# Performance work log

Measured on AMD Instinct MI355X. Metric: run time of the kernel, lower is better.

Reference implementation:

```python
import jax, jax.numpy as jnp
import numpy as np
from jax import lax

LAG, K, DIM, HEADS, HID, CLASSES = 8192, 4, 1024, 16, 5, 2
PRICE = 9 - K  # cat((output[k], prices)) must have length 9 (LSTM input_size)


def setup_inputs() -> dict:
    key = jax.random.key(0)
    ks = jax.random.split(key, 30)
    n = lambda i, shape, s=1.0: jax.random.normal(ks[i], shape, jnp.float32) * s
    w = 0.02  # weight init scale for stability
    return {
        "text": n(0, (LAG, K, DIM)),
        "prices": n(1, (LAG, PRICE)),
        "pos_embed": n(2, (LAG, K, DIM), w),
        "Wq1": n(3, (DIM, DIM), w), "Wk1": n(4, (DIM, DIM), w),
        "Wv1": n(5, (DIM, DIM), w), "Wo1": n(6, (DIM, DIM), w),
        "ln_g": jnp.ones((DIM,), jnp.float32), "ln_b": jnp.zeros((DIM,), jnp.float32),
        "W1": n(7, (DIM, DIM), w), "b1": jnp.zeros((DIM,), jnp.float32),
        "W2": n(8, (DIM, DIM), w), "b2": jnp.zeros((DIM,), jnp.float32),
        "Wq2": n(9, (DIM, DIM), w), "Wk2": n(10, (DIM, DIM), w),
        "Wv2": n(11, (DIM, DIM), w), "Wo2": n(12, (DIM, DIM), w),
        "w_u": n(13, (DIM, DIM)), "w_m": n(14, (DIM,)),
        "Wih": n(15, (4 * HID, 9), 0.3), "Whh": n(16, (4 * HID, HID), 0.3),
        "bih": jnp.zeros((4 * HID,), jnp.float32), "bhh": jnp.zeros((4 * HID,), jnp.float32),
        "Wt": n(17, (9 + HID, CLASSES), 0.3), "bt": jnp.zeros((CLASSES,), jnp.float32),
        "Wa": n(18, (9 + HID, CLASSES), 0.3), "ba": jnp.zeros((CLASSES,), jnp.float32),
    }


def _mha(x, Wq, Wk, Wv, Wo, h):
    # x: [lag, k, d]; batched multi-head self-attention over the k axis
    L, k, d = x.shape
    dh = d // h
    q = (x @ Wq).reshape(L, k, h, dh)
    kk = (x @ Wk).reshape(L, k, h, dh)
    v = (x @ Wv).reshape(L, k, h, dh)
    s = jnp.einsum('lqhd,lkhd->lhqk', q, kk) / jnp.sqrt(jnp.float32(dh))
    a = jax.nn.softmax(s, axis=-1)
    o = jnp.einsum('lhqk,lkhd->lqhd', a, v).reshape(L, k, d)
    return o @ Wo


def _layernorm(x, g, b, eps=1e-5):
    mu = jnp.mean(x, axis=-1, keepdims=True)
    var = jnp.mean(jnp.square(x - mu), axis=-1, keepdims=True)
    return (x - mu) * lax.rsqrt(var + eps) * g + b


def reference(text, prices, pos_embed, Wq1, Wk1, Wv1, Wo1, ln_g, ln_b,
              W1, b1, W2, b2, Wq2, Wk2, Wv2, Wo2, w_u, w_m,
              Wih, Whh, bih, bhh, Wt, bt, Wa, ba):
    # input[0] += pos_embed, then per-tweet textEncoder -- vectorized over lag
    x = text + pos_embed                                   # [lag, k, d]
    inter = _mha(x, Wq1, Wk1, Wv1, Wo1, HEADS)             # multi-head attn
    y = _layernorm(inter + x, ln_g, ln_b)                  # residual + LN
    ffn = jax.nn.relu(y @ W1 + b1) @ W2 + b2               # FFN
    m = _mha(ffn, Wq2, Wk2, Wv2, Wo2, 1)                   # single-head attn -> [lag, k, d]
    # inter = softmax(w_u^T @ tanh(w_m)) is constant across the loop
    att = jax.nn.softmax(w_u.T @ jnp.tanh(w_m), axis=0)    # [d]
    out_k = jnp.einsum('lkd,d->lk', m, att)                # [lag, k]
    lstm_in = jnp.concatenate([out_k, prices], axis=1)     # [lag, 9]

    # single-layer LSTM (pytorch gate order i, f, g, o), h0 = c0 = 0
    def step(carry, xt):
        h, c = carry
        g = xt @ Wih.T + h @ Whh.T + bih + bhh
        i, f, gg, o = jnp.split(g, 4)
        c = jax.nn.sigmoid(f) * c + jax.nn.sigmoid(i) * jnp.tanh(gg)
        h = jax.nn.sigmoid(o) * jnp.tanh(c)
        return (h, c), h

    init = (jnp.zeros((HID,), lstm_in.dtype), jnp.zeros((HID,), lstm_in.dtype))
    _, hs = lax.scan(step, init, lstm_in)                  # [lag, 5]

    feat = jnp.concatenate([lstm_in, hs], axis=1)          # [lag, 14]
    final = feat @ Wt + bt                                 # [lag, num_classes]
    auxiliary = feat @ Wa + ba                             # [lag, num_classes]
    return final, auxiliary
```

## Files before the change

kernel.cpp:

```cpp
#include <hip/hip_runtime.h>
#include <hip/hip_bf16.h>
#include <math.h>

#define LAG   8192
#define NROW  32768
#define DIMD  1024

typedef __attribute__((ext_vector_type(8))) short  short8;
typedef __attribute__((ext_vector_type(4))) float  f32x4;
typedef __attribute__((ext_vector_type(2))) float  f32x2;
typedef unsigned short ushort_t;
typedef unsigned int   uint_t;

__device__ __forceinline__ uint_t split2_pack(float f) {
    unsigned u = __float_as_uint(f);
    unsigned r = u + 0x7FFFu + ((u >> 16) & 1u);
    unsigned h = r >> 16;
    float hf = __uint_as_float(h << 16);
    float lf = f - hf;
    unsigned u2 = __float_as_uint(lf);
    unsigned r2 = u2 + 0x7FFFu + ((u2 >> 16) & 1u);
    return h | (r2 & 0xFFFF0000u);
}
__device__ __forceinline__ float updp(uint_t p) {
    return __uint_as_float(p << 16) + __uint_as_float(p & 0xFFFF0000u);
}

__device__ __forceinline__ void unpack16(const uint_t* r, uint4& h0, uint4& h1,
                                         uint4& l0, uint4& l1) {
    h0.x = __builtin_amdgcn_perm(r[1],  r[0],  0x05040100u);
    h0.y = __builtin_amdgcn_perm(r[3],  r[2],  0x05040100u);
    h0.z = __builtin_amdgcn_perm(r[5],  r[4],  0x05040100u);
    h0.w = __builtin_amdgcn_perm(r[7],  r[6],  0x05040100u);
    h1.x = __builtin_amdgcn_perm(r[9],  r[8],  0x05040100u);
    h1.y = __builtin_amdgcn_perm(r[11], r[10], 0x05040100u);
    h1.z = __builtin_amdgcn_perm(r[13], r[12], 0x05040100u);
    h1.w = __builtin_amdgcn_perm(r[15], r[14], 0x05040100u);
    l0.x = __builtin_amdgcn_perm(r[1],  r[0],  0x07060302u);
    l0.y = __builtin_amdgcn_perm(r[3],  r[2],  0x07060302u);
    l0.z = __builtin_amdgcn_perm(r[5],  r[4],  0x07060302u);
    l0.w = __builtin_amdgcn_perm(r[7],  r[6],  0x07060302u);
    l1.x = __builtin_amdgcn_perm(r[9],  r[8],  0x07060302u);
    l1.y = __builtin_amdgcn_perm(r[11], r[10], 0x07060302u);
    l1.z = __builtin_amdgcn_perm(r[13], r[12], 0x07060302u);
    l1.w = __builtin_amdgcn_perm(r[15], r[14], 0x07060302u);
}

template<int BM, int CM, bool BIAS, bool RELU>
__global__ __launch_bounds__(256) void mgemm(
    const uint_t* __restrict__ Apk, const void* __restrict__ Bsrc,
    const float* __restrict__ bias,
    float* __restrict__ Cf, uint_t* __restrict__ Cp)
{
    __shared__ ushort_t As_h[128*40], As_l[128*40], Bs_h[128*40], Bs_l[128*40];
    const int tid  = threadIdx.x;
    const int lane = tid & 63;
    const int wave = tid >> 6;
    const int wm   = (wave & 1) * 64;
    const int wn   = (wave >> 1) * 64;
    const int ln15 = lane & 15;
    const int q8   = (lane >> 4) * 8;
    const int lin  = blockIdx.y * 8 + blockIdx.x;
    const int swz  = (lin & 7) * gridDim.y + (lin >> 3);
    const int row0 = (swz >> 3) * 128;
    const int col0 = (swz & 7) * 128;

    const int ar  = tid >> 1;
    const int ako = (tid & 1) << 4;
    const int bn  = tid & 127;
    const int bk  = (tid >> 7) << 4;

    f32x4 acc[4][4] = {};

    uint_t a_r[16] __attribute__((aligned(16)));
    uint_t b_r[16] __attribute__((aligned(16)));

    {
        const uint_t* Apt = Apk + (size_t)(row0 + ar) * DIMD + ako;
        *(uint4*)&a_r[0]  = *(const uint4*)(Apt + 0);
        *(uint4*)&a_r[4]  = *(const uint4*)(Apt + 4);
        *(uint4*)&a_r[8]  = *(const uint4*)(Apt + 8);
        *(uint4*)&a_r[12] = *(const uint4*)(Apt + 12);
        if constexpr (BM == 1) {
            const uint_t* Bpt = (const uint_t*)Bsrc + (size_t)bk * DIMD + col0 + bn;
            #pragma unroll
            for (int i = 0; i < 16; ++i) b_r[i] = Bpt[(size_t)i * DIMD];
        } else {
            const float* Bpt = (const float*)Bsrc + (size_t)bk * DIMD + col0 + bn;
            #pragma unroll
            for (int i = 0; i < 16; ++i) b_r[i] = split2_pack(Bpt[(size_t)i * DIMD]);
        }
    }

    for (int k0 = 0; k0 < DIMD; k0 += 32) {
        __syncthreads();
        {
            uint4 h0, h1, l0, l1;
            unpack16(a_r, h0, h1, l0, l1);
            *(uint4*)&As_h[ar*40 + ako]     = h0;
            *(uint4*)&As_h[ar*40 + ako + 8] = h1;
            *(uint4*)&As_l[ar*40 + ako]     = l0;
            *(uint4*)&As_l[ar*40 + ako + 8] = l1;
            unpack16(b_r, h0, h1, l0, l1);
            *(uint4*)&Bs_h[bn*40 + bk]      = h0;
            *(uint4*)&Bs_h[bn*40 + bk + 8]  = h1;
            *(uint4*)&Bs_l[bn*40 + bk]      = l0;
            *(uint4*)&Bs_l[bn*40 + bk + 8]  = l1;
        }
        __syncthreads();

        if (k0 + 32 < DIMD) {
            const int kn = k0 + 32;
            const uint_t* Apt = Apk + (size_t)(row0 + ar) * DIMD + kn + ako;
            *(uint4*)&a_r[0]  = *(const uint4*)(Apt + 0);
            *(uint4*)&a_r[4]  = *(const uint4*)(Apt + 4);
            *(uint4*)&a_r[8]  = *(const uint4*)(Apt + 8);
            *(uint4*)&a_r[12] = *(const uint4*)(Apt + 12);
            if constexpr (BM == 1) {
                const uint_t* Bpt = (const uint_t*)Bsrc + (size_t)(kn + bk) * DIMD + col0 + bn;
                #pragma unroll
                for (int i = 0; i < 16; ++i) b_r[i] = Bpt[(size_t)i * DIMD];
            } else {
                const float* Bpt = (const float*)Bsrc + (size_t)(kn + bk) * DIMD + col0 + bn;
                #pragma unroll
                for (int i = 0; i < 16; ++i) b_r[i] = split2_pack(Bpt[(size_t)i * DIMD]);
            }
        }

        short8 fah[4], fal[4];
        #pragma unroll
        for (int i = 0; i < 4; ++i) {
            fah[i] = *(const short8*)&As_h[(wm + 16*i + ln15)*40 + q8];
            fal[i] = *(const short8*)&As_l[(wm + 16*i + ln15)*40 + q8];
        }
        #pragma unroll
        for (int j = 0; j < 4; ++j) {
            short8 fbh = *(const short8*)&Bs_h[(wn + 16*j + ln15)*40 + q8];
            short8 fbl = *(const short8*)&Bs_l[(wn + 16*j + ln15)*40 + q8];
            #pragma unroll
            for (int i = 0; i < 4; ++i) {
                acc[i][j] = __builtin_amdgcn_mfma_f32_16x16x32_bf16(fal[i], fbh, acc[i][j], 0, 0, 0);
                acc[i][j] = __builtin_amdgcn_mfma_f32_16x16x32_bf16(fah[i], fbl, acc[i][j], 0, 0, 0);
                acc[i][j] = __builtin_amdgcn_mfma_f32_16x16x32_bf16(fah[i], fbh, acc[i][j], 0, 0, 0);
            }
        }
    }

    #pragma unroll
    for (int j = 0; j < 4; ++j) {
        const int col = col0 + wn + 16*j + ln15;
        float bv = 0.f;
        if constexpr (BIAS) bv = bias[col];
        #pragma unroll
        for (int i = 0; i < 4; ++i) {
            #pragma unroll
            for (int r = 0; r < 4; ++r) {
                const int row = row0 + wm + 16*i + (lane >> 4)*4 + r;
                float v = acc[i][j][r] + bv;
                if constexpr (RELU) v = fmaxf(v, 0.f);
                if constexpr (CM == 0) Cf[(size_t)row*DIMD + col] = v;
                else                   Cp[(size_t)row*DIMD + col] = split2_pack(v);
            }
        }
    }
}

template<bool TRANS_B>
__global__ __launch_bounds__(256) void gemm_f32(
    const float* __restrict__ A, const float* __restrict__ B, float* __restrict__ C)
{
    __shared__ float As[16][132];
    __shared__ float Bs[16][132];
    const int tid  = threadIdx.x;
    const int tx   = tid & 15;
    const int ty   = tid >> 4;
    const int row0 = blockIdx.y * 128;
    const int col0 = blockIdx.x * 128;

    float acc[8][8];
    #pragma unroll
    for (int i = 0; i < 8; ++i)
        #pragma unroll
        for (int j = 0; j < 8; ++j) acc[i][j] = 0.f;

    for (int k0 = 0; k0 < DIMD; k0 += 16) {
        #pragma unroll
        for (int t = 0; t < 2; ++t) {
            int i  = tid + t * 256;
            int arr = i >> 2, ak = (i & 3) << 2;
            float4 av = *(const float4*)(A + (size_t)(row0 + arr) * DIMD + k0 + ak);
            As[ak + 0][arr] = av.x; As[ak + 1][arr] = av.y;
            As[ak + 2][arr] = av.z; As[ak + 3][arr] = av.w;
            if constexpr (TRANS_B) {
                float4 bv4 = *(const float4*)(B + (size_t)(col0 + arr) * DIMD + k0 + ak);
                Bs[ak + 0][arr] = bv4.x; Bs[ak + 1][arr] = bv4.y;
                Bs[ak + 2][arr] = bv4.z; Bs[ak + 3][arr] = bv4.w;
            } else {
                int br = i >> 5, bc = (i & 31) << 2;
                *(float4*)&Bs[br][bc] =
                    *(const float4*)(B + (size_t)(k0 + br) * DIMD + col0 + bc);
            }
        }
        __syncthreads();
        #pragma unroll
        for (int kk = 0; kk < 16; ++kk) {
            float a[8], b[8];
            *(float4*)&a[0] = *(const float4*)&As[kk][ty * 8];
            *(float4*)&a[4] = *(const float4*)&As[kk][ty * 8 + 4];
            *(float4*)&b[0] = *(const float4*)&Bs[kk][tx * 4];
            *(float4*)&b[4] = *(const float4*)&Bs[kk][64 + tx * 4];
            #pragma unroll
            for (int i = 0; i < 8; ++i)
                #pragma unroll
                for (int j = 0; j < 8; ++j)
                    acc[i][j] = fmaf(a[i], b[j], acc[i][j]);
        }
        __syncthreads();
    }
    #pragma unroll
    for (int i = 0; i < 8; ++i) {
        size_t rr = (size_t)(row0 + ty * 8 + i) * DIMD;
        *(float4*)(C + rr + col0 + tx * 4)      = *(float4*)&acc[i][0];
        *(float4*)(C + rr + col0 + 64 + tx * 4) = *(float4*)&acc[i][4];
    }
}

__global__ __launch_bounds__(256) void mv_kernel(
    const float* __restrict__ W, const float* __restrict__ x,
    float* __restrict__ y)
{
    const int row  = blockIdx.x * 4 + (threadIdx.x >> 6);
    const int lane = threadIdx.x & 63;
    float a = 0.f;
    #pragma unroll
    for (int c = 0; c < 16; ++c) {
        int off = c * 64 + lane;
        a = fmaf(W[(size_t)row * DIMD + off], x[off], a);
    }
    #pragma unroll
    for (int d = 1; d < 64; d <<= 1) a += __shfl_xor(a, d);
    if (lane == 0) y[row] = a;
}

__global__ __launch_bounds__(1024) void mvt_part_kernel(
    const float* __restrict__ W, const float* __restrict__ x,
    float* __restrict__ part)
{
    const int b   = blockIdx.x;
    const int tid = threadIdx.x;
    float a = 0.f;
    #pragma unroll 4
    for (int j = b * 64; j < b * 64 + 64; ++j)
        a = fmaf(W[(size_t)j * DIMD + tid], x[j], a);
    part[(size_t)b * DIMD + tid] = a;
}
__global__ __launch_bounds__(256) void mvt_red_kernel(
    const float* __restrict__ part, float* __restrict__ y)
{
    const int i = blockIdx.x * 256 + threadIdx.x;
    float s = 0.f;
    #pragma unroll
    for (int c = 0; c < 16; ++c) s += part[(size_t)c * DIMD + i];
    y[i] = s;
}

__global__ __launch_bounds__(1024) void dot_kernel(
    const float* __restrict__ a, const float* __restrict__ b,
    float* __restrict__ out)
{
    __shared__ float red[16];
    const int tid = threadIdx.x;
    float p = a[tid] * b[tid];
    #pragma unroll
    for (int d = 1; d < 64; d <<= 1) p += __shfl_xor(p, d);
    if ((tid & 63) == 0) red[tid >> 6] = p;
    __syncthreads();
    if (tid < 16) {
        float x = red[tid];
        #pragma unroll
        for (int d = 1; d < 16; d <<= 1) x += __shfl_xor(x, d);
        if (tid == 0) out[0] = x;
    }
}

__global__ __launch_bounds__(256) void splitw_kernel(
    const float* __restrict__ in, uint_t* __restrict__ out)
{
    const size_t i = ((size_t)blockIdx.x * 256 + threadIdx.x) * 4;
    float4 v = *(const float4*)(in + i);
    uint4 o;
    o.x = split2_pack(v.x); o.y = split2_pack(v.y);
    o.z = split2_pack(v.z); o.w = split2_pack(v.w);
    *(uint4*)(out + i) = o;
}

__global__ __launch_bounds__(256) void splitwt_kernel(
    const float* __restrict__ in, uint_t* __restrict__ out)
{
    const int tid = blockIdx.x * 256 + threadIdx.x;
    const int k   = tid & 1023;
    const int n0  = (tid >> 10) << 2;
    uint4 o;
    o.x = split2_pack(in[(size_t)(n0 + 0) * DIMD + k]);
    o.y = split2_pack(in[(size_t)(n0 + 1) * DIMD + k]);
    o.z = split2_pack(in[(size_t)(n0 + 2) * DIMD + k]);
    o.w = split2_pack(in[(size_t)(n0 + 3) * DIMD + k]);
    *(uint4*)(out + (size_t)k * DIMD + n0) = o;
}

__global__ __launch_bounds__(256) void splitx_kernel(
    const float* __restrict__ text, const float* __restrict__ pos,
    uint_t* __restrict__ out)
{
    const size_t i = ((size_t)blockIdx.x * 256 + threadIdx.x) * 4;
    float4 a = *(const float4*)(text + i);
    float4 b = *(const float4*)(pos + i);
    uint4 o;
    o.x = split2_pack(a.x + b.x); o.y = split2_pack(a.y + b.y);
    o.z = split2_pack(a.z + b.z); o.w = split2_pack(a.w + b.w);
    *(uint4*)(out + i) = o;
}

__global__ __launch_bounds__(256) void score_kernel(
    const uint_t* __restrict__ q, const uint_t* __restrict__ k,
    float* __restrict__ prob)
{
    const int l    = blockIdx.x;
    const int qi   = threadIdx.x >> 6;
    const int lane = threadIdx.x & 63;
    const size_t base = (size_t)l * 4 * DIMD;
    const float scale = 0.125f;

    #pragma unroll 1
    for (int h = 0; h < 16; ++h) {
        int off = h * 64 + lane;
        float qv = updp(q[base + qi * DIMD + off]);
        float s0 = qv * updp(k[base + 0 * DIMD + off]);
        float s1 = qv * updp(k[base + 1 * DIMD + off]);
        float s2 = qv * updp(k[base + 2 * DIMD + off]);
        float s3 = qv * updp(k[base + 3 * DIMD + off]);
        #pragma unroll
        for (int d = 1; d < 64; d <<= 1) {
            s0 += __shfl_xor(s0, d);
            s1 += __shfl_xor(s1, d);
            s2 += __shfl_xor(s2, d);
            s3 += __shfl_xor(s3, d);
        }
        s0 *= scale; s1 *= scale; s2 *= scale; s3 *= scale;
        float mx = fmaxf(fmaxf(s0, s1), fmaxf(s2, s3));
        float e0 = expf(s0 - mx), e1 = expf(s1 - mx);
        float e2 = expf(s2 - mx), e3 = expf(s3 - mx);
        float inv = 1.f / (e0 + e1 + e2 + e3);
        if (lane == 0) {
            float4 p = { e0 * inv, e1 * inv, e2 * inv, e3 * inv };
            *(float4*)&prob[(((size_t)l * 4 + qi) * 16 + h) * 4] = p;
        }
    }
}

__global__ __launch_bounds__(256) void mixln_kernel(
    const uint_t* __restrict__ vmat, const float* __restrict__ prob,
    const float* __restrict__ text, const float* __restrict__ pos,
    const float* __restrict__ g, const float* __restrict__ b,
    uint_t* __restrict__ yp)
{
    const int l    = blockIdx.x;
    const int qi   = threadIdx.x >> 6;
    const int lane = threadIdx.x & 63;
    const size_t base  = (size_t)l * 4 * DIMD;
    const size_t rbase = base + (size_t)qi * DIMD;
    float v[16];
    float s = 0.f;
    #pragma unroll
    for (int c = 0; c < 16; ++c) {
        int off = c * 64 + lane;
        float4 p = *(const float4*)&prob[(((size_t)l * 4 + qi) * 16 + c) * 4];
        float r = p.x * updp(vmat[base + 0 * DIMD + off])
                + p.y * updp(vmat[base + 1 * DIMD + off])
                + p.z * updp(vmat[base + 2 * DIMD + off])
                + p.w * updp(vmat[base + 3 * DIMD + off]);
        v[c] = r + text[rbase + off] + pos[rbase + off];
        s += v[c];
    }
    #pragma unroll
    for (int d = 1; d < 64; d <<= 1) s += __shfl_xor(s, d);
    float mu = s * (1.f / 1024.f);
    float vs = 0.f;
    #pragma unroll
    for (int c = 0; c < 16; ++c) { float t = v[c] - mu; vs += t * t; }
    #pragma unroll
    for (int d = 1; d < 64; d <<= 1) vs += __shfl_xor(vs, d);
    float rs = rsqrtf(vs * (1.f / 1024.f) + 1e-5f);
    #pragma unroll
    for (int c = 0; c < 16; ++c) {
        int off = c * 64 + lane;
        float y = (v[c] - mu) * rs * g[off] + b[off];
        yp[rbase + off] = split2_pack(y);
    }
}

__global__ __launch_bounds__(256) void attn2out_kernel(
    const uint_t* __restrict__ xp, const float* __restrict__ t,
    const float* __restrict__ wvec2, const float* __restrict__ czv,
    const float* __restrict__ prices,
    const float* __restrict__ Wih, const float* __restrict__ bih,
    const float* __restrict__ bhh,
    float* __restrict__ lstm_in, float* __restrict__ pre)
{
    const int l    = blockIdx.x;
    const int qi   = threadIdx.x >> 6;
    const int lane = threadIdx.x & 63;
    const size_t base = (size_t)l * 4 * DIMD;
    __shared__ float li[9];

    float s0 = 0.f, s1 = 0.f, s2 = 0.f, s3 = 0.f;
    float z0 = 0.f, z1 = 0.f, z2 = 0.f, z3 = 0.f;
    #pragma unroll
    for (int c = 0; c < 16; ++c) {
        int off = c * 64 + lane;
        float tv = t[base + qi * DIMD + off];
        float wv = wvec2[off];
        float x0 = updp(xp[base + 0 * DIMD + off]);
        float x1 = updp(xp[base + 1 * DIMD + off]);
        float x2 = updp(xp[base + 2 * DIMD + off]);
        float x3 = updp(xp[base + 3 * DIMD + off]);
        s0 = fmaf(tv, x0, s0); z0 = fmaf(wv, x0, z0);
        s1 = fmaf(tv, x1, s1); z1 = fmaf(wv, x1, z1);
        s2 = fmaf(tv, x2, s2); z2 = fmaf(wv, x2, z2);
        s3 = fmaf(tv, x3, s3); z3 = fmaf(wv, x3, z3);
    }
    #pragma unroll
    for (int d = 1; d < 64; d <<= 1) {
        s0 += __shfl_xor(s0, d); s1 += __shfl_xor(s1, d);
        s2 += __shfl_xor(s2, d); s3 += __shfl_xor(s3, d);
        z0 += __shfl_xor(z0, d); z1 += __shfl_xor(z1, d);
        z2 += __shfl_xor(z2, d); z3 += __shfl_xor(z3, d);
    }
    const float cz = czv[0];
    z0 += cz; z1 += cz; z2 += cz; z3 += cz;
    const float scale = 0.03125f;
    s0 *= scale; s1 *= scale; s2 *= scale; s3 *= scale;
    float mx = fmaxf(fmaxf(s0, s1), fmaxf(s2, s3));
    float e0 = expf(s0 - mx), e1 = expf(s1 - mx);
    float e2 = expf(s2 - mx), e3 = expf(s3 - mx);
    float inv = 1.f / (e0 + e1 + e2 + e3);
    float ok = (e0 * z0 + e1 * z1 + e2 * z2 + e3 * z3) * inv;

    if (lane == 0) li[qi] = ok;
    if (threadIdx.x >= 64 && threadIdx.x < 69)
        li[4 + threadIdx.x - 64] = prices[(size_t)l * 5 + threadIdx.x - 64];
    __syncthreads();
    if (threadIdx.x < 9) lstm_in[(size_t)l * 9 + threadIdx.x] = li[threadIdx.x];
    if (threadIdx.x < 20) {
        int gg = threadIdx.x;
        float p = bih[gg] + bhh[gg];
        #pragma unroll
        for (int j = 0; j < 9; ++j) p = fmaf(li[j], Wih[gg * 9 + j], p);
        pre[(size_t)l * 20 + (gg % 5) * 4 + (gg / 5)] = p;
    }
}

__global__ __launch_bounds__(1024) void att_kernel(
    const float* __restrict__ w_u, const float* __restrict__ w_m,
    float* __restrict__ att)
{
    __shared__ float tj[1024];
    __shared__ float red[16];
    const int tid = threadIdx.x;
    tj[tid] = tanhf(w_m[tid]);
    __syncthreads();
    float a = 0.f;
    #pragma unroll 8
    for (int j = 0; j < 1024; ++j)
        a = fmaf(w_u[(size_t)j * 1024 + tid], tj[j], a);
    float m = a;
    #pragma unroll
    for (int d = 1; d < 64; d <<= 1) m = fmaxf(m, __shfl_xor(m, d));
    if ((tid & 63) == 0) red[tid >> 6] = m;
    __syncthreads();
    if (tid < 16) {
        float x = red[tid];
        #pragma unroll
        for (int d = 1; d < 16; d <<= 1) x = fmaxf(x, __shfl_xor(x, d));
        red[tid] = x;
    }
    __syncthreads();
    float mx = red[0];
    float e = expf(a - mx);
    float s = e;
    #pragma unroll
    for (int d = 1; d < 64; d <<= 1) s += __shfl_xor(s, d);
    __syncthreads();
    if ((tid & 63) == 0) red[tid >> 6] = s;
    __syncthreads();
    if (tid < 16) {
        float x = red[tid];
        #pragma unroll
        for (int d = 1; d < 16; d <<= 1) x += __shfl_xor(x, d);
        red[tid] = x;
    }
    __syncthreads();
    att[tid] = e / red[0];
}

#define LCHUNK 256
#define LWARM  512

__device__ __forceinline__ float bcast(float x, int srclane) {
    return __uint_as_float(__builtin_amdgcn_readlane(__float_as_uint(x), srclane));
}
__device__ __forceinline__ float fsig(float x) {
    return __builtin_amdgcn_rcpf(1.f + __expf(-x));
}
__device__ __forceinline__ float ftanh(float x) {
    float e = __expf(-2.f * x);
    return (1.f - e) * __builtin_amdgcn_rcpf(1.f + e);
}

__global__ __launch_bounds__(64) void lstm_kernel(
    const float* __restrict__ pre, const float* __restrict__ Whh,
    float* __restrict__ hs)
{
    const int lane = threadIdx.x;
    const int m    = (lane < 5) ? lane : 0;
    const int blk  = blockIdx.x;
    const int cbase  = blk * LCHUNK;
    const int base   = (cbase >= LWARM) ? cbase - LWARM : 0;
    const int skip   = cbase - base;
    const int nsteps = skip + LCHUNK;

    f32x2 wif[5], wgo[5];
    #pragma unroll
    for (int j = 0; j < 5; ++j) {
        wif[j] = (f32x2){ Whh[( 0 + m) * 5 + j], Whh[( 5 + m) * 5 + j] };
        wgo[j] = (f32x2){ Whh[(10 + m) * 5 + j], Whh[(15 + m) * 5 + j] };
    }
    float cm = 0.f, hm = 0.f;
    float s0 = 0.f, s1 = 0.f, s2 = 0.f, s3 = 0.f, s4 = 0.f;

    float4 buf[16];
    #pragma unroll
    for (int j = 0; j < 16; ++j)
        buf[j] = *(const float4*)(pre + (size_t)(base + j) * 20 + m * 4);

    #define LSTM_STEP(j, EMIT)                                                  \
        {                                                                       \
            float4 p = buf[j];                                                  \
            buf[j] = *(const float4*)(pre + (size_t)(base + l0 + 16 + (j)) * 20 + m * 4); \
            f32x2 S0 = { s0, s0 }, S1 = { s1, s1 }, S2 = { s2, s2 };            \
            f32x2 S3 = { s3, s3 }, S4 = { s4, s4 };                             \
            f32x2 gif = { p.x, p.y };                                           \
            f32x2 ggo = { p.z, p.w };                                           \
            f32x2 t1 = S0 * wif[0] + gif;                                       \
            f32x2 t2 = S1 * wif[1] + S2 * wif[2];                               \
            f32x2 t3 = S3 * wif[3] + S4 * wif[4];                               \
            gif = t1 + t2 + t3;                                                 \
            f32x2 u1 = S0 * wgo[0] + ggo;                                       \
            f32x2 u2 = S1 * wgo[1] + S2 * wgo[2];                               \
            f32x2 u3 = S3 * wgo[3] + S4 * wgo[4];                               \
            ggo = u1 + u2 + u3;                                                 \
            float si = fsig(gif.x);                                             \
            float sf = fsig(gif.y);                                             \
            float tg = ftanh(ggo.x);                                            \
            float so = fsig(ggo.y);                                             \
            cm = fmaf(sf, cm, si * tg);                                         \
            hm = so * ftanh(cm);                                                \
            if (EMIT) hs[(size_t)(base + l0 + (j)) * 5 + m] = hm;               \
            s0 = bcast(hm, 0); s1 = bcast(hm, 1); s2 = bcast(hm, 2);            \
            s3 = bcast(hm, 3); s4 = bcast(hm, 4);                               \
        }

    int l0 = 0;
    for (; l0 < skip; l0 += 16) {
        #pragma unroll
        for (int j = 0; j < 16; ++j) LSTM_STEP(j, false)
    }
    for (; l0 < nsteps; l0 += 16) {
        #pragma unroll
        for (int j = 0; j < 16; ++j) LSTM_STEP(j, true)
    }
    #undef LSTM_STEP
}

__global__ __launch_bounds__(256) void final_kernel(
    const float* __restrict__ lstm_in, const float* __restrict__ hs,
    const float* __restrict__ Wt, const float* __restrict__ bt,
    const float* __restrict__ Wa, const float* __restrict__ ba,
    float* __restrict__ out)
{
    const int l = blockIdx.x * 256 + threadIdx.x;
    float f[14];
    #pragma unroll
    for (int j = 0; j < 9; ++j) f[j] = lstm_in[(size_t)l * 9 + j];
    #pragma unroll
    for (int j = 0; j < 5; ++j) f[9 + j] = hs[(size_t)l * 5 + j];
    #pragma unroll
    for (int c = 0; c < 2; ++c) {
        float a = bt[c], b = ba[c];
        #pragma unroll
        for (int j = 0; j < 14; ++j) {
            a = fmaf(f[j], Wt[j * 2 + c], a);
            b = fmaf(f[j], Wa[j * 2 + c], b);
        }
        out[(size_t)l * 2 + c]         = a;
        out[16384 + (size_t)l * 2 + c] = b;
    }
}

extern "C" void kernel_launch(void* const* d_in, const int* in_sizes, int n_in,
                              void* d_out, int out_size, void* d_ws, size_t ws_size,
                              hipStream_t stream)
{
    const float* text   = (const float*)d_in[0];
    const float* prices = (const float*)d_in[1];
    const float* pos    = (const float*)d_in[2];
    const float* Wq1    = (const float*)d_in[3];
    const float* Wk1    = (const float*)d_in[4];
    const float* Wv1    = (const float*)d_in[5];
    const float* Wo1    = (const float*)d_in[6];
    const float* ln_g   = (const float*)d_in[7];
    const float* ln_b   = (const float*)d_in[8];
    const float* W1     = (const float*)d_in[9];
    const float* b1     = (const float*)d_in[10];
    const float* W2     = (const float*)d_in[11];
    const float* b2     = (const float*)d_in[12];
    const float* Wq2    = (const float*)d_in[13];
    const float* Wk2    = (const float*)d_in[14];
    const float* Wv2    = (const float*)d_in[15];
    const float* Wo2    = (const float*)d_in[16];
    const float* w_u    = (const float*)d_in[17];
    const float* w_m    = (const float*)d_in[18];
    const float* Wih    = (const float*)d_in[19];
    const float* Whh    = (const float*)d_in[20];
    const float* bih    = (const float*)d_in[21];
    const float* bhh    = (const float*)d_in[22];
    const float* Wt     = (const float*)d_in[23];
    const float* bt     = (const float*)d_in[24];
    const float* Wa     = (const float*)d_in[25];
    const float* ba     = (const float*)d_in[26];

    float* ws = (float*)d_ws;
    const size_t BUF = (size_t)NROW * DIMD;
    const size_t MW  = (size_t)DIMD * DIMD;
    float* A = ws;
    float* B = ws + BUF;
    float* C = ws + 2 * BUF;
    float* F0   = ws + 3 * BUF;
    float* F1   = F0 + MW;
    float* attL = F1 + MW;
    float* U    = attL + 1024;
    float* prob    = U;
    float* lstm_in = U;
    float* pre     = lstm_in + (size_t)LAG * 9;
    float* hs      = pre + ((size_t)LAG * 20 + 400);
    uint_t* Wpk    = (uint_t*)(U + 2097152);
    float* out     = (float*)d_out;

    const size_t need_base = ((size_t)(3 * BUF) + 2 * MW + 1024 + 2097152) * 4;
    const size_t need_full = need_base + 8 * MW * 4;
    const bool full = ws_size >= need_full;

    uint_t* Ap = (uint_t*)A;
    uint_t* Bp = (uint_t*)B;
    uint_t* Cp = (uint_t*)C;

    uint_t* S0 = Wpk + 0 * MW;  uint_t* S1 = Wpk + 1 * MW;
    uint_t* S2 = Wpk + 2 * MW;  uint_t* S3 = Wpk + 3 * MW;
    uint_t* S4 = Wpk + 4 * MW;  uint_t* S6 = Wpk + 6 * MW;
    uint_t* S7 = Wpk + 7 * MW;
    float* vecs = full ? (float*)(Wpk + 5 * MW) : (float*)Wpk;
    float* attS  = vecs;
    float* tmpS  = vecs + 1024;
    float* wvec  = vecs + 2048;
    float* wvec2 = vecs + 3072;
    float* w_a   = vecs + 4096;
    float* w_b   = vecs + 5120;
    float* vv    = vecs + 6144;
    float* czv   = vecs + 7168;
    float* partS = vecs + 8192;

    dim3 ggrid(8, 256), gblk(256);
    dim3 pgrid(8, 8);

    att_kernel<<<1, 1024, 0, stream>>>(w_u, w_m, attS);
    mv_kernel<<<256, 256, 0, stream>>>(Wo2, attS, tmpS);
    mv_kernel<<<256, 256, 0, stream>>>(Wv2, tmpS, wvec);
    mv_kernel<<<256, 256, 0, stream>>>(W2, wvec, wvec2);
    dot_kernel<<<1, 1024, 0, stream>>>(b2, wvec, czv);
    mvt_part_kernel<<<16, 1024, 0, stream>>>(Wq2, b2, partS);
    mvt_red_kernel<<<4, 256, 0, stream>>>(partS, w_a);
    mv_kernel<<<256, 256, 0, stream>>>(Wk2, w_a, w_b);
    mv_kernel<<<256, 256, 0, stream>>>(W2, w_b, vv);

    splitx_kernel<<<32768, 256, 0, stream>>>(text, pos, Ap);

    if (full) {
        splitw_kernel<<<1024, 256, 0, stream>>>(W2,  S6);
        splitw_kernel<<<1024, 256, 0, stream>>>(Wq2, S7);
        mgemm<1,0,false,false><<<pgrid, gblk, 0, stream>>>(S6, S7, nullptr, F0, nullptr);
        splitw_kernel<<<1024, 256, 0, stream>>>(Wk2, S7);
        mgemm<1,0,false,false><<<pgrid, gblk, 0, stream>>>(S6, S7, nullptr, F1, nullptr);
        splitw_kernel <<<1024, 256, 0, stream>>>(F0, S6);
        splitwt_kernel<<<1024, 256, 0, stream>>>(F1, S7);
        mgemm<1,0,false,false><<<pgrid, gblk, 0, stream>>>(S6, S7, nullptr, F0, nullptr);
        splitw_kernel<<<1024, 256, 0, stream>>>(F0, S3);
        splitw_kernel<<<1024, 256, 0, stream>>>(Wv1, S6);
        splitw_kernel<<<1024, 256, 0, stream>>>(Wo1, S7);
        mgemm<1,0,false,false><<<pgrid, gblk, 0, stream>>>(S6, S7, nullptr, F1, nullptr);
        splitw_kernel<<<1024, 256, 0, stream>>>(F1, S4);
        splitw_kernel<<<1024, 256, 0, stream>>>(Wq1, S0);
        splitw_kernel<<<1024, 256, 0, stream>>>(Wk1, S1);
        splitw_kernel<<<1024, 256, 0, stream>>>(W1,  S2);

        mgemm<1,1,false,false><<<ggrid, gblk, 0, stream>>>(Ap, S0, nullptr, nullptr, Bp);
        mgemm<1,1,false,false><<<ggrid, gblk, 0, stream>>>(Ap, S1, nullptr, nullptr, Cp);
        score_kernel<<<LAG, 256, 0, stream>>>(Bp, Cp, prob);
        mgemm<1,1,false,false><<<ggrid, gblk, 0, stream>>>(Ap, S4, nullptr, nullptr, Bp);
        mixln_kernel<<<LAG, 256, 0, stream>>>(Bp, prob, text, pos, ln_g, ln_b, Cp);
        mgemm<1,1,true ,true ><<<ggrid, gblk, 0, stream>>>(Cp, S2, b1, nullptr, Bp);
        mgemm<1,0,true ,false><<<ggrid, gblk, 0, stream>>>(Bp, S3, vv, A, nullptr);
    } else {
        gemm_f32<false><<<pgrid, gblk, 0, stream>>>(W2, Wq2, U);
        gemm_f32<false><<<pgrid, gblk, 0, stream>>>(W2, Wk2, U + MW);
        gemm_f32<true ><<<pgrid, gblk, 0, stream>>>(U, U + MW, F0);
        gemm_f32<false><<<pgrid, gblk, 0, stream>>>(Wv1, Wo1, F1);

        mgemm<0,1,false,false><<<ggrid, gblk, 0, stream>>>(Ap, Wq1, nullptr, nullptr, Bp);
        mgemm<0,1,false,false><<<ggrid, gblk, 0, stream>>>(Ap, Wk1, nullptr, nullptr, Cp);
        score_kernel<<<LAG, 256, 0, stream>>>(Bp, Cp, prob);
        mgemm<0,1,false,false><<<ggrid, gblk, 0, stream>>>(Ap, F1,  nullptr, nullptr, Bp);
        mixln_kernel<<<LAG, 256, 0, stream>>>(Bp, prob, text, pos, ln_g, ln_b, Cp);
        mgemm<0,1,true ,true ><<<ggrid, gblk, 0, stream>>>(Cp, W1,  b1, nullptr, Bp);
        mgemm<0,0,true ,false><<<ggrid, gblk, 0, stream>>>(Bp, F0,  vv, A, nullptr);
    }

    attn2out_kernel<<<LAG, 256, 0, stream>>>(Bp, A, wvec2, czv, prices,
                                             Wih, bih, bhh, lstm_in, pre);

    lstm_kernel <<<32, 64, 0, stream>>>(pre, Whh, hs);
    final_kernel<<<32, 256, 0, stream>>>(lstm_in, hs, Wt, bt, Wa, ba, out);
}
```

Measured before the change: 2.059 ms.

## Add 256x256-tile split-bf16 MFMA GEMM with planar hi/lo layout

```diff
diff --git a/kernel.cpp b/kernel.cpp
--- a/kernel.cpp
+++ b/kernel.cpp
@@ -24,6 +24,9 @@
 }
 __device__ __forceinline__ float updp(uint_t p) {
     return __uint_as_float(p << 16) + __uint_as_float(p & 0xFFFF0000u);
+}
+__device__ __forceinline__ float up2(ushort_t h, ushort_t l) {
+    return __uint_as_float((uint_t)h << 16) + __uint_as_float((uint_t)l << 16);
 }
 
 __device__ __forceinline__ void unpack16(const uint_t* r, uint4& h0, uint4& h1,
@@ -46,6 +49,173 @@
     l1.w = __builtin_amdgcn_perm(r[15], r[14], 0x07060302u);
 }
 
+#define NT8 48
+
+template<int CM, bool BIAS, bool RELU>
+__global__ __launch_bounds__(512, 2) void gemm8(
+    const ushort_t* __restrict__ Ah, const ushort_t* __restrict__ Al,
+    const ushort_t* __restrict__ Bth, const ushort_t* __restrict__ Btl,
+    const float* __restrict__ bias,
+    float* __restrict__ Cf, ushort_t* __restrict__ Ch, ushort_t* __restrict__ Cl)
+{
+    __shared__ ushort_t lds8[65536];
+    const int tid  = threadIdx.x;
+    const int lane = tid & 63;
+    const int wave = tid >> 6;
+    const int wr   = wave >> 2;
+    const int wc   = wave & 3;
+    const int ln15 = lane & 15;
+    const int g    = lane >> 4;
+
+    const int lin  = blockIdx.y * 4 + blockIdx.x;
+    const int cpx  = gridDim.y >> 1;
+    const int swz  = (lin & 7) * cpx + (lin >> 3);
+    const int row0 = (swz >> 2) * 256;
+    const int col0 = (swz & 3) * 256;
+
+    const int sr   = tid >> 3;
+    const int sch  = tid & 7;
+    const int woff0 = sr * 64 + ((sch ^ (sr & 7)) * 8);
+    const int fx0 = ((g)     ^ (ln15 & 7)) * 8;
+    const int fx1 = ((4 + g) ^ (ln15 & 7)) * 8;
+
+    f32x4 acc[8][4] = {};
+    uint4 st[4][2];
+
+#define G8_LOAD(tt)                                                             \
+    {                                                                           \
+        const int seg_ = (tt) >> 4;                                             \
+        const int ko_  = ((tt) & 15) * 64;                                      \
+        const ushort_t* ap_ = (seg_ == 2) ? Al  : Ah;                           \
+        const ushort_t* bp_ = (seg_ == 1) ? Btl : Bth;                          \
+        st[0][0] = *(const uint4*)(ap_ + (size_t)(row0 +       sr) * DIMD + ko_ + sch * 8); \
+        st[0][1] = *(const uint4*)(ap_ + (size_t)(row0 +  64 + sr) * DIMD + ko_ + sch * 8); \
+        st[1][0] = *(const uint4*)(ap_ + (size_t)(row0 + 128 + sr) * DIMD + ko_ + sch * 8); \
+        st[1][1] = *(const uint4*)(ap_ + (size_t)(row0 + 192 + sr) * DIMD + ko_ + sch * 8); \
+        st[2][0] = *(const uint4*)(bp_ + (size_t)(col0 +       sr) * DIMD + ko_ + sch * 8); \
+        st[2][1] = *(const uint4*)(bp_ + (size_t)(col0 +  64 + sr) * DIMD + ko_ + sch * 8); \
+        st[3][0] = *(const uint4*)(bp_ + (size_t)(col0 + 128 + sr) * DIMD + ko_ + sch * 8); \
+        st[3][1] = *(const uint4*)(bp_ + (size_t)(col0 + 192 + sr) * DIMD + ko_ + sch * 8); \
+    }
+#define G8_WRITE(bb)                                                            \
+    {                                                                           \
+        ushort_t* d_ = lds8 + (bb) * 32768;                                     \
+        *(uint4*)&d_[0 * 8192 + woff0]        = st[0][0];                       \
+        *(uint4*)&d_[0 * 8192 + woff0 + 4096] = st[0][1];                       \
+        *(uint4*)&d_[1 * 8192 + woff0]        = st[1][0];                       \
+        *(uint4*)&d_[1 * 8192 + woff0 + 4096] = st[1][1];                       \
+        *(uint4*)&d_[2 * 8192 + woff0]        = st[2][0];                       \
+        *(uint4*)&d_[2 * 8192 + woff0 + 4096] = st[2][1];                       \
+        *(uint4*)&d_[3 * 8192 + woff0]        = st[3][0];                       \
+        *(uint4*)&d_[3 * 8192 + woff0 + 4096] = st[3][1];                       \
+    }
+
+    G8_LOAD(0);
+    G8_WRITE(0);
+    G8_LOAD(1);
+    asm volatile("s_waitcnt lgkmcnt(0)" ::: "memory");
+    __builtin_amdgcn_s_barrier();
+    __builtin_amdgcn_sched_barrier(0);
+
+    for (int t = 0; t < NT8; ++t) {
+        const int b = t & 1;
+        if (t + 1 < NT8) G8_WRITE(1 - b);
+        if (t + 2 < NT8) G8_LOAD(t + 2);
+
+        const ushort_t* Lb = lds8 + b * 32768;
+        short8 af[4][2], bf0[2][2], bf1[2][2];
+        #pragma unroll
+        for (int i = 0; i < 4; ++i) {
+            int rr = (2 * i + wr) * 16 + ln15;
+            af[i][0] = *(const short8*)&Lb[rr * 64 + fx0];
+            af[i][1] = *(const short8*)&Lb[rr * 64 + fx1];
+        }
+        #pragma unroll
+        for (int j = 0; j < 2; ++j) {
+            int rr = (4 * j + wc) * 16 + ln15;
+            bf0[j][0] = *(const short8*)&Lb[2 * 8192 + rr * 64 + fx0];
+            bf0[j][1] = *(const short8*)&Lb[2 * 8192 + rr * 64 + fx1];
+        }
+        __builtin_amdgcn_s_setprio(1);
+        #pragma unroll
+        for (int i = 0; i < 4; ++i)
+            #pragma unroll
+            for (int j = 0; j < 2; ++j) {
+                acc[i][j] = __builtin_amdgcn_mfma_f32_16x16x32_bf16(af[i][0], bf0[j][0], acc[i][j], 0, 0, 0);
+                acc[i][j] = __builtin_amdgcn_mfma_f32_16x16x32_bf16(af[i][1], bf0[j][1], acc[i][j], 0, 0, 0);
+            }
+        __builtin_amdgcn_s_setprio(0);
+        #pragma unroll
+        for (int j = 0; j < 2; ++j) {
+            int rr = (4 * j + wc) * 16 + ln15;
+            bf1[j][0] = *(const short8*)&Lb[3 * 8192 + rr * 64 + fx0];
+            bf1[j][1] = *(const short8*)&Lb[3 * 8192 + rr * 64 + fx1];
+        }
+        __builtin_amdgcn_s_setprio(1);
+        #pragma unroll
+        for (int i = 0; i < 4; ++i)
+            #pragma unroll
+            for (int j = 0; j < 2; ++j) {
+                acc[i][2 + j] = __builtin_amdgcn_mfma_f32_16x16x32_bf16(af[i][0], bf1[j][0], acc[i][2 + j], 0, 0, 0);
+                acc[i][2 + j] = __builtin_amdgcn_mfma_f32_16x16x32_bf16(af[i][1], bf1[j][1], acc[i][2 + j], 0, 0, 0);
+            }
+        __builtin_amdgcn_s_setprio(0);
+        #pragma unroll
+        for (int i = 0; i < 4; ++i) {
+            int rr = (2 * i + wr) * 16 + ln15;
+            af[i][0] = *(const short8*)&Lb[1 * 8192 + rr * 64 + fx0];
+            af[i][1] = *(const short8*)&Lb[1 * 8192 + rr * 64 + fx1];
+        }
+        __builtin_amdgcn_s_setprio(1);
+        #pragma unroll
+        for (int i = 0; i < 4; ++i)
+            #pragma unroll
+            for (int j = 0; j < 2; ++j) {
+                acc[4 + i][j] = __builtin_amdgcn_mfma_f32_16x16x32_bf16(af[i][0], bf0[j][0], acc[4 + i][j], 0, 0, 0);
+                acc[4 + i][j] = __builtin_amdgcn_mfma_f32_16x16x32_bf16(af[i][1], bf0[j][1], acc[4 + i][j], 0, 0, 0);
+            }
+        #pragma unroll
+        for (int i = 0; i < 4; ++i)
+            #pragma unroll
+            for (int j = 0; j < 2; ++j) {
+                acc[4 + i][2 + j] = __builtin_amdgcn_mfma_f32_16x16x32_bf16(af[i][0], bf1[j][0], acc[4 + i][2 + j], 0, 0, 0);
+                acc[4 + i][2 + j] = __builtin_amdgcn_mfma_f32_16x16x32_bf16(af[i][1], bf1[j][1], acc[4 + i][2 + j], 0, 0, 0);
+            }
+        __builtin_amdgcn_s_setprio(0);
+
+        asm volatile("s_waitcnt lgkmcnt(0)" ::: "memory");
+        __builtin_amdgcn_sched_barrier(0);
+        __builtin_amdgcn_s_barrier();
+        __builtin_amdgcn_sched_barrier(0);
+    }
+#undef G8_LOAD
+#undef G8_WRITE
+
+    #pragma unroll
+    for (int J = 0; J < 4; ++J) {
+        const int col = col0 + ((J >> 1) * 8 + (J & 1) * 4 + wc) * 16 + ln15;
+        float bv = 0.f;
+        if constexpr (BIAS) bv = bias[col];
+        #pragma unroll
+        for (int I = 0; I < 8; ++I) {
+            const int srow = (I >> 2) * 8 + 2 * (I & 3) + wr;
+            #pragma unroll
+            for (int r = 0; r < 4; ++r) {
+                const int row = row0 + srow * 16 + g * 4 + r;
+                float v = acc[I][J][r] + bv;
+                if constexpr (RELU) v = fmaxf(v, 0.f);
+                if constexpr (CM == 0) {
+                    Cf[(size_t)row * DIMD + col] = v;
+                } else {
+                    uint_t p = split2_pack(v);
+                    Ch[(size_t)row * DIMD + col] = (ushort_t)(p & 0xFFFFu);
+                    Cl[(size_t)row * DIMD + col] = (ushort_t)(p >> 16);
+                }
+            }
+        }
+    }
+}
+
 template<int BM, int CM, bool BIAS, bool RELU>
 __global__ __launch_bounds__(256) void mgemm(
     const uint_t* __restrict__ Apk, const void* __restrict__ Bsrc,
@@ -283,29 +453,55 @@
     }
 }
 
-__global__ __launch_bounds__(256) void splitw_kernel(
-    const float* __restrict__ in, uint_t* __restrict__ out)
+__global__ __launch_bounds__(256) void splitw2(
+    const float* __restrict__ in, ushort_t* __restrict__ oh, ushort_t* __restrict__ ol)
 {
     const size_t i = ((size_t)blockIdx.x * 256 + threadIdx.x) * 4;
     float4 v = *(const float4*)(in + i);
-    uint4 o;
-    o.x = split2_pack(v.x); o.y = split2_pack(v.y);
-    o.z = split2_pack(v.z); o.w = split2_pack(v.w);
-    *(uint4*)(out + i) = o;
-}
-
-__global__ __launch_bounds__(256) void splitwt_kernel(
-    const float* __restrict__ in, uint_t* __restrict__ out)
-{
-    const int tid = blockIdx.x * 256 + threadIdx.x;
-    const int k   = tid & 1023;
-    const int n0  = (tid >> 10) << 2;
-    uint4 o;
-    o.x = split2_pack(in[(size_t)(n0 + 0) * DIMD + k]);
-    o.y = split2_pack(in[(size_t)(n0 + 1) * DIMD + k]);
-    o.z = split2_pack(in[(size_t)(n0 + 2) * DIMD + k]);
-    o.w = split2_pack(in[(size_t)(n0 + 3) * DIMD + k]);
-    *(uint4*)(out + (size_t)k * DIMD + n0) = o;
+    uint_t p0 = split2_pack(v.x), p1 = split2_pack(v.y);
+    uint_t p2 = split2_pack(v.z), p3 = split2_pack(v.w);
+    uint2 h, l;
+    h.x = (p0 & 0xFFFFu) | (p1 << 16);        h.y = (p2 & 0xFFFFu) | (p3 << 16);
+    l.x = (p0 >> 16)     | (p1 & 0xFFFF0000u); l.y = (p2 >> 16)    | (p3 & 0xFFFF0000u);
+    *(uint2*)(oh + i) = h;
+    *(uint2*)(ol + i) = l;
+}
+
+__global__ __launch_bounds__(256) void splitwt2(
+    const float* __restrict__ in, ushort_t* __restrict__ oh, ushort_t* __restrict__ ol)
+{
+    __shared__ float tile[64][65];
+    const int bx = blockIdx.x & 15;
+    const int by = blockIdx.x >> 4;
+    const int c  = threadIdx.x & 63;
+    const int r4 = threadIdx.x >> 6;
+    #pragma unroll
+    for (int rr = 0; rr < 64; rr += 4)
+        tile[rr + r4][c] = in[(size_t)(by * 64 + rr + r4) * DIMD + bx * 64 + c];
+    __syncthreads();
+    #pragma unroll
+    for (int rr = 0; rr < 64; rr += 4) {
+        uint_t p = split2_pack(tile[c][rr + r4]);
+        size_t o = (size_t)(bx * 64 + rr + r4) * DIMD + by * 64 + c;
+        oh[o] = (ushort_t)(p & 0xFFFFu);
+        ol[o] = (ushort_t)(p >> 16);
+    }
+}
+
+__global__ __launch_bounds__(256) void splitx2(
+    const float* __restrict__ text, const float* __restrict__ pos,
+    ushort_t* __restrict__ oh, ushort_t* __restrict__ ol)
+{
+    const size_t i = ((size_t)blockIdx.x * 256 + threadIdx.x) * 4;
+    float4 a = *(const float4*)(text + i);
+    float4 b = *(const float4*)(pos + i);
+    uint_t p0 = split2_pack(a.x + b.x), p1 = split2_pack(a.y + b.y);
+    uint_t p2 = split2_pack(a.z + b.z), p3 = split2_pack(a.w + b.w);
+    uint2 h, l;
+    h.x = (p0 & 0xFFFFu) | (p1 << 16);        h.y = (p2 & 0xFFFFu) | (p3 << 16);
+    l.x = (p0 >> 16)     | (p1 & 0xFFFF0000u); l.y = (p2 >> 16)    | (p3 & 0xFFFF0000u);
+    *(uint2*)(oh + i) = h;
+    *(uint2*)(ol + i) = l;
 }
 
 __global__ __launch_bounds__(256) void splitx_kernel(
@@ -319,6 +515,44 @@
     o.x = split2_pack(a.x + b.x); o.y = split2_pack(a.y + b.y);
     o.z = split2_pack(a.z + b.z); o.w = split2_pack(a.w + b.w);
     *(uint4*)(out + i) = o;
+}
+
+__global__ __launch_bounds__(256) void score2(
+    const ushort_t* __restrict__ qh, const ushort_t* __restrict__ ql,
+    const ushort_t* __restrict__ kh, const ushort_t* __restrict__ kl,
+    float* __restrict__ prob)
+{
+    const int l    = blockIdx.x;
+    const int qi   = threadIdx.x >> 6;
+    const int lane = threadIdx.x & 63;
+    const size_t base = (size_t)l * 4 * DIMD;
+    const float scale = 0.125f;
+
+    #pragma unroll 1
+    for (int h = 0; h < 16; ++h) {
+        int off = h * 64 + lane;
+        float qv = up2(qh[base + qi * DIMD + off], ql[base + qi * DIMD + off]);
+        float s0 = qv * up2(kh[base + 0 * DIMD + off], kl[base + 0 * DIMD + off]);
+        float s1 = qv * up2(kh[base + 1 * DIMD + off], kl[base + 1 * DIMD + off]);
+        float s2 = qv * up2(kh[base + 2 * DIMD + off], kl[base + 2 * DIMD + off]);
+        float s3 = qv * up2(kh[base + 3 * DIMD + off], kl[base + 3 * DIMD + off]);
+        #pragma unroll
+        for (int d = 1; d < 64; d <<= 1) {
+            s0 += __shfl_xor(s0, d);
+            s1 += __shfl_xor(s1, d);
+            s2 += __shfl_xor(s2, d);
+            s3 += __shfl_xor(s3, d);
+        }
+        s0 *= scale; s1 *= scale; s2 *= scale; s3 *= scale;
+        float mx = fmaxf(fmaxf(s0, s1), fmaxf(s2, s3));
+        float e0 = expf(s0 - mx), e1 = expf(s1 - mx);
+        float e2 = expf(s2 - mx), e3 = expf(s3 - mx);
+        float inv = 1.f / (e0 + e1 + e2 + e3);
+        if (lane == 0) {
+            float4 p = { e0 * inv, e1 * inv, e2 * inv, e3 * inv };
+            *(float4*)&prob[(((size_t)l * 4 + qi) * 16 + h) * 4] = p;
+        }
+    }
 }
 
 __global__ __launch_bounds__(256) void score_kernel(
@@ -355,6 +589,50 @@
             float4 p = { e0 * inv, e1 * inv, e2 * inv, e3 * inv };
             *(float4*)&prob[(((size_t)l * 4 + qi) * 16 + h) * 4] = p;
         }
+    }
+}
+
+__global__ __launch_bounds__(256) void mixln2(
+    const ushort_t* __restrict__ vh, const ushort_t* __restrict__ vl,
+    const float* __restrict__ prob,
+    const float* __restrict__ text, const float* __restrict__ pos,
+    const float* __restrict__ g, const float* __restrict__ b,
+    ushort_t* __restrict__ yh, ushort_t* __restrict__ yl)
+{
+    const int l    = blockIdx.x;
+    const int qi   = threadIdx.x >> 6;
+    const int lane = threadIdx.x & 63;
+    const size_t base  = (size_t)l * 4 * DIMD;
+    const size_t rbase = base + (size_t)qi * DIMD;
+    float v[16];
+    float s = 0.f;
+    #pragma unroll
+    for (int c = 0; c < 16; ++c) {
+        int off = c * 64 + lane;
+        float4 p = *(const float4*)&prob[(((size_t)l * 4 + qi) * 16 + c) * 4];
+        float r = p.x * up2(vh[base + 0 * DIMD + off], vl[base + 0 * DIMD + off])
+                + p.y * up2(vh[base + 1 * DIMD + off], vl[base + 1 * DIMD + off])
+                + p.z * up2(vh[base + 2 * DIMD + off], vl[base + 2 * DIMD + off])
+                + p.w * up2(vh[base + 3 * DIMD + off], vl[base + 3 * DIMD + off]);
+        v[c] = r + text[rbase + off] + pos[rbase + off];
+        s += v[c];
+    }
+    #pragma unroll
+    for (int d = 1; d < 64; d <<= 1) s += __shfl_xor(s, d);
+    float mu = s * (1.f / 1024.f);
+    float vs = 0.f;
+    #pragma unroll
+    for (int c = 0; c < 16; ++c) { float t = v[c] - mu; vs += t * t; }
+    #pragma unroll
+    for (int d = 1; d < 64; d <<= 1) vs += __shfl_xor(vs, d);
+    float rs = rsqrtf(vs * (1.f / 1024.f) + 1e-5f);
+    #pragma unroll
+    for (int c = 0; c < 16; ++c) {
+        int off = c * 64 + lane;
+        float y = (v[c] - mu) * rs * g[off] + b[off];
+        uint_t p = split2_pack(y);
+        yh[rbase + off] = (ushort_t)(p & 0xFFFFu);
+        yl[rbase + off] = (ushort_t)(p >> 16);
     }
 }
 
@@ -396,6 +674,68 @@
         int off = c * 64 + lane;
         float y = (v[c] - mu) * rs * g[off] + b[off];
         yp[rbase + off] = split2_pack(y);
+    }
+}
+
+__global__ __launch_bounds__(256) void attn2out2(
+    const ushort_t* __restrict__ xh, const ushort_t* __restrict__ xl,
+    const float* __restrict__ t,
+    const float* __restrict__ wvec2, const float* __restrict__ czv,
+    const float* __restrict__ prices,
+    const float* __restrict__ Wih, const float* __restrict__ bih,
+    const float* __restrict__ bhh,
+    float* __restrict__ lstm_in, float* __restrict__ pre)
+{
+    const int l    = blockIdx.x;
+    const int qi   = threadIdx.x >> 6;
+    const int lane = threadIdx.x & 63;
+    const size_t base = (size_t)l * 4 * DIMD;
+    __shared__ float li[9];
+
+    float s0 = 0.f, s1 = 0.f, s2 = 0.f, s3 = 0.f;
+    float z0 = 0.f, z1 = 0.f, z2 = 0.f, z3 = 0.f;
+    #pragma unroll
+    for (int c = 0; c < 16; ++c) {
+        int off = c * 64 + lane;
+        float tv = t[base + qi * DIMD + off];
+        float wv = wvec2[off];
+        float x0 = up2(xh[base + 0 * DIMD + off], xl[base + 0 * DIMD + off]);
+        float x1 = up2(xh[base + 1 * DIMD + off], xl[base + 1 * DIMD + off]);
+        float x2 = up2(xh[base + 2 * DIMD + off], xl[base + 2 * DIMD + off]);
+        float x3 = up2(xh[base + 3 * DIMD + off], xl[base + 3 * DIMD + off]);
+        s0 = fmaf(tv, x0, s0); z0 = fmaf(wv, x0, z0);
+        s1 = fmaf(tv, x1, s1); z1 = fmaf(wv, x1, z1);
+        s2 = fmaf(tv, x2, s2); z2 = fmaf(wv, x2, z2);
+        s3 = fmaf(tv, x3, s3); z3 = fmaf(wv, x3, z3);
+    }
+    #pragma unroll
+    for (int d = 1; d < 64; d <<= 1) {
+        s0 += __shfl_xor(s0, d); s1 += __shfl_xor(s1, d);
+        s2 += __shfl_xor(s2, d); s3 += __shfl_xor(s3, d);
+        z0 += __shfl_xor(z0, d); z1 += __shfl_xor(z1, d);
+        z2 += __shfl_xor(z2, d); z3 += __shfl_xor(z3, d);
+    }
+    const float cz = czv[0];
+    z0 += cz; z1 += cz; z2 += cz; z3 += cz;
+    const float scale = 0.03125f;
+    s0 *= scale; s1 *= scale; s2 *= scale; s3 *= scale;
+    float mx = fmaxf(fmaxf(s0, s1), fmaxf(s2, s3));
+    float e0 = expf(s0 - mx), e1 = expf(s1 - mx);
+    float e2 = expf(s2 - mx), e3 = expf(s3 - mx);
+    float inv = 1.f / (e0 + e1 + e2 + e3);
+    float ok = (e0 * z0 + e1 * z1 + e2 * z2 + e3 * z3) * inv;
+
+    if (lane == 0) li[qi] = ok;
+    if (threadIdx.x >= 64 && threadIdx.x < 69)
+        li[4 + threadIdx.x - 64] = prices[(size_t)l * 5 + threadIdx.x - 64];
+    __syncthreads();
+    if (threadIdx.x < 9) lstm_in[(size_t)l * 9 + threadIdx.x] = li[threadIdx.x];
+    if (threadIdx.x < 20) {
+        int gg = threadIdx.x;
+        float p = bih[gg] + bhh[gg];
+        #pragma unroll
+        for (int j = 0; j < 9; ++j) p = fmaf(li[j], Wih[gg * 9 + j], p);
+        pre[(size_t)l * 20 + (gg % 5) * 4 + (gg / 5)] = p;
     }
 }
 
@@ -664,10 +1004,16 @@
     uint_t* Bp = (uint_t*)B;
     uint_t* Cp = (uint_t*)C;
 
+    ushort_t* Axh = (ushort_t*)A;  ushort_t* Axl = Axh + BUF;
+    ushort_t* Bxh = (ushort_t*)B;  ushort_t* Bxl = Bxh + BUF;
+    ushort_t* Cxh = (ushort_t*)C;  ushort_t* Cxl = Cxh + BUF;
+
     uint_t* S0 = Wpk + 0 * MW;  uint_t* S1 = Wpk + 1 * MW;
     uint_t* S2 = Wpk + 2 * MW;  uint_t* S3 = Wpk + 3 * MW;
     uint_t* S4 = Wpk + 4 * MW;  uint_t* S6 = Wpk + 6 * MW;
     uint_t* S7 = Wpk + 7 * MW;
+#define PH(s) ((ushort_t*)(s))
+#define PL(s) ((ushort_t*)(s) + MW)
     float* vecs = full ? (float*)(Wpk + 5 * MW) : (float*)Wpk;
     float* attS  = vecs;
     float* tmpS  = vecs + 1024;
@@ -679,6 +1025,7 @@
     float* czv   = vecs + 7168;
     float* partS = vecs + 8192;
 
+    dim3 gbig(4, 128), gsml(4, 4), gblk8(512);
     dim3 ggrid(8, 256), gblk(256);
     dim3 pgrid(8, 8);
 
@@ -692,34 +1039,47 @@
     mv_kernel<<<256, 256, 0, stream>>>(Wk2, w_a, w_b);
     mv_kernel<<<256, 256, 0, stream>>>(W2, w_b, vv);
 
-    splitx_kernel<<<32768, 256, 0, stream>>>(text, pos, Ap);
-
     if (full) {
-        splitw_kernel<<<1024, 256, 0, stream>>>(W2,  S6);
-        splitw_kernel<<<1024, 256, 0, stream>>>(Wq2, S7);
-        mgemm<1,0,false,false><<<pgrid, gblk, 0, stream>>>(S6, S7, nullptr, F0, nullptr);
-        splitw_kernel<<<1024, 256, 0, stream>>>(Wk2, S7);
-        mgemm<1,0,false,false><<<pgrid, gblk, 0, stream>>>(S6, S7, nullptr, F1, nullptr);
-        splitw_kernel <<<1024, 256, 0, stream>>>(F0, S6);
-        splitwt_kernel<<<1024, 256, 0, stream>>>(F1, S7);
-        mgemm<1,0,false,false><<<pgrid, gblk, 0, stream>>>(S6, S7, nullptr, F0, nullptr);
-        splitw_kernel<<<1024, 256, 0, stream>>>(F0, S3);
-        splitw_kernel<<<1024, 256, 0, stream>>>(Wv1, S6);
-        splitw_kernel<<<1024, 256, 0, stream>>>(Wo1, S7);
-        mgemm<1,0,false,false><<<pgrid, gblk, 0, stream>>>(S6, S7, nullptr, F1, nullptr);
-        splitw_kernel<<<1024, 256, 0, stream>>>(F1, S4);
-        splitw_kernel<<<1024, 256, 0, stream>>>(Wq1, S0);
-        splitw_kernel<<<1024, 256, 0, stream>>>(Wk1, S1);
-        splitw_kernel<<<1024, 256, 0, stream>>>(W1,  S2);
-
-        mgemm<1,1,false,false><<<ggrid, gblk, 0, stream>>>(Ap, S0, nullptr, nullptr, Bp);
-        mgemm<1,1,false,false><<<ggrid, gblk, 0, stream>>>(Ap, S1, nullptr, nullptr, Cp);
-        score_kernel<<<LAG, 256, 0, stream>>>(Bp, Cp, prob);
-        mgemm<1,1,false,false><<<ggrid, gblk, 0, stream>>>(Ap, S4, nullptr, nullptr, Bp);
-        mixln_kernel<<<LAG, 256, 0, stream>>>(Bp, prob, text, pos, ln_g, ln_b, Cp);
-        mgemm<1,1,true ,true ><<<ggrid, gblk, 0, stream>>>(Cp, S2, b1, nullptr, Bp);
-        mgemm<1,0,true ,false><<<ggrid, gblk, 0, stream>>>(Bp, S3, vv, A, nullptr);
+        splitx2<<<32768, 256, 0, stream>>>(text, pos, Axh, Axl);
+
+        splitw2 <<<1024, 256, 0, stream>>>(W2,  PH(S6), PL(S6));
+        splitwt2<<<256, 256, 0, stream>>>(Wq2, PH(S7), PL(S7));
+        gemm8<0,false,false><<<gsml, gblk8, 0, stream>>>(PH(S6), PL(S6), PH(S7), PL(S7),
+                                                         nullptr, F0, nullptr, nullptr);
+        splitwt2<<<256, 256, 0, stream>>>(Wk2, PH(S7), PL(S7));
+        gemm8<0,false,false><<<gsml, gblk8, 0, stream>>>(PH(S6), PL(S6), PH(S7), PL(S7),
+                                                         nullptr, F1, nullptr, nullptr);
+        splitw2<<<1024, 256, 0, stream>>>(F0, PH(S6), PL(S6));
+        splitw2<<<1024, 256, 0, stream>>>(F1, PH(S7), PL(S7));
+        gemm8<0,false,false><<<gsml, gblk8, 0, stream>>>(PH(S6), PL(S6), PH(S7), PL(S7),
+                                                         nullptr, F0, nullptr, nullptr);
+        splitwt2<<<256, 256, 0, stream>>>(F0, PH(S3), PL(S3));
+        splitw2 <<<1024, 256, 0, stream>>>(Wv1, PH(S6), PL(S6));
+        splitwt2<<<256, 256, 0, stream>>>(Wo1, PH(S7), PL(S7));
+        gemm8<0,false,false><<<gsml, gblk8, 0, stream>>>(PH(S6), PL(S6), PH(S7), PL(S7),
+                                                         nullptr, F1, nullptr, nullptr);
+        splitwt2<<<256, 256, 0, stream>>>(F1, PH(S4), PL(S4));
+        splitwt2<<<256, 256, 0, stream>>>(Wq1, PH(S0), PL(S0));
+        splitwt2<<<256, 256, 0, stream>>>(Wk1, PH(S1), PL(S1));
+        splitwt2<<<256, 256, 0, stream>>>(W1,  PH(S2), PL(S2));
+
+        gemm8<1,false,false><<<gbig, gblk8, 0, stream>>>(Axh, Axl, PH(S0), PL(S0),
+                                                         nullptr, nullptr, Bxh, Bxl);
+        gemm8<1,false,false><<<gbig, gblk8, 0, stream>>>(Axh, Axl, PH(S1), PL(S1),
+                                                         nullptr, nullptr, Cxh, Cxl);
+        score2<<<LAG, 256, 0, stream>>>(Bxh, Bxl, Cxh, Cxl, prob);
+        gemm8<1,false,false><<<gbig, gblk8, 0, stream>>>(Axh, Axl, PH(S4), PL(S4),
+                                                         nullptr, nullptr, Bxh, Bxl);
+        mixln2<<<LAG, 256, 0, stream>>>(Bxh, Bxl, prob, text, pos, ln_g, ln_b,
+                                        Cxh, Cxl);
+        gemm8<1,true ,true ><<<gbig, gblk8, 0, stream>>>(Cxh, Cxl, PH(S2), PL(S2),
+                                                         b1, nullptr, Bxh, Bxl);
+        gemm8<0,true ,false><<<gbig, gblk8, 0, stream>>>(Bxh, Bxl, PH(S3), PL(S3),
+                                                         vv, A, nullptr, nullptr);
+        attn2out2<<<LAG, 256, 0, stream>>>(Bxh, Bxl, A, wvec2, czv, prices,
+                                           Wih, bih, bhh, lstm_in, pre);
     } else {
+        splitx_kernel<<<32768, 256, 0, stream>>>(text, pos, Ap);
         gemm_f32<false><<<pgrid, gblk, 0, stream>>>(W2, Wq2, U);
         gemm_f32<false><<<pgrid, gblk, 0, stream>>>(W2, Wk2, U + MW);
         gemm_f32<true ><<<pgrid, gblk, 0, stream>>>(U, U + MW, F0);
@@ -732,10 +1092,9 @@
         mixln_kernel<<<LAG, 256, 0, stream>>>(Bp, prob, text, pos, ln_g, ln_b, Cp);
         mgemm<0,1,true ,true ><<<ggrid, gblk, 0, stream>>>(Cp, W1,  b1, nullptr, Bp);
         mgemm<0,0,true ,false><<<ggrid, gblk, 0, stream>>>(Bp, F0,  vv, A, nullptr);
-    }
-
-    attn2out_kernel<<<LAG, 256, 0, stream>>>(Bp, A, wvec2, czv, prices,
-                                             Wih, bih, bhh, lstm_in, pre);
+        attn2out_kernel<<<LAG, 256, 0, stream>>>(Bp, A, wvec2, czv, prices,
+                                                 Wih, bih, bhh, lstm_in, pre);
+    }
 
     lstm_kernel <<<32, 64, 0, stream>>>(pre, Whh, hs);
     final_kernel<<<32, 256, 0, stream>>>(lstm_in, hs, Wt, bt, Wa, ba, out);
```

Measured after the change: 4.724 ms. +129.4%, slower.
